# Kernel tuning notes

Measured on AMD Instinct MI355X. Metric: run time of the kernel, lower is better.

The kernel has to match this reference:

```python
import jax, jax.numpy as jnp
import numpy as np

B_SZ, SEQ, D_MODEL = 1, 2048, 1024
D_IN, N_STATE, DT_RANK, KSIZE = 2048, 16, 64, 3


def setup_inputs() -> dict:
    key = jax.random.key(0)
    ks = jax.random.split(key, 7)
    x = jax.random.normal(ks[0], (B_SZ, SEQ, D_MODEL), jnp.float32)
    W_in = jax.random.normal(ks[1], (D_MODEL, 2 * D_IN), jnp.float32) * 0.02
    conv_w = jax.random.normal(ks[2], (D_IN, 1, KSIZE), jnp.float32) * 0.1  # OIH, depthwise
    W_x = jax.random.normal(ks[3], (D_IN, DT_RANK + 2 * N_STATE), jnp.float32) * 0.02
    W_delta = jax.random.normal(ks[4], (DT_RANK, D_IN), jnp.float32) * 0.02
    b_delta = jnp.zeros((D_IN,), jnp.float32)
    # Keras initializer: A_log[d, n] = n+1 (arange 1..N repeated over d_in rows)
    A_log = jnp.tile(jnp.arange(1, N_STATE + 1, dtype=jnp.float32)[None, :], (D_IN, 1))
    D = jnp.ones((D_IN,), jnp.float32)
    W_out = jax.random.normal(ks[5], (D_IN, D_MODEL), jnp.float32) * 0.02
    return dict(x=x, W_in=W_in, conv_w=conv_w, W_x=W_x, W_delta=W_delta,
                b_delta=b_delta, A_log=A_log, D=D, W_out=W_out)


def selective_scan(u, delta, A, Bm, Cm, D):
    # u, delta: (b,l,d); A: (d,n); Bm, Cm: (b,l,n); D: (d,)
    dA = jnp.einsum('bld,dn->bldn', delta, A)
    dB_u = jnp.einsum('bld,bld,bln->bldn', delta, u, Bm)
    # shift dA left by one step, zero at the end (matches pad+slice in source)
    dA_shift = jnp.concatenate([dA[:, 1:], jnp.zeros_like(dA[:, :1])], axis=1)
    # reversed cumulative sum along time, then exp
    dA_cs = jnp.exp(jnp.flip(jnp.cumsum(jnp.flip(dA_shift, axis=1), axis=1), axis=1))
    xs = jnp.cumsum(dB_u * dA_cs, axis=1) / (dA_cs + 1e-12)
    y = jnp.einsum('bldn,bln->bld', xs, Cm)
    return y + u * D


def reference(x, W_in, conv_w, W_x, W_delta, b_delta, A_log, D, W_out):
    d_in = conv_w.shape[0]
    ksz = conv_w.shape[2]
    n = A_log.shape[1]
    dtr = W_delta.shape[0]
    x_and_res = x @ W_in                       # (b,l,2*d_in)
    xi, res = x_and_res[..., :d_in], x_and_res[..., d_in:]
    # depthwise causal conv over time (channels_first with left padding k-1)
    xc = jnp.transpose(xi, (0, 2, 1))          # (b,d_in,l)
    xc = jax.lax.conv_general_dilated(
        xc, conv_w, window_strides=(1,), padding=[(ksz - 1, 0)],
        dimension_numbers=('NCH', 'OIH', 'NCH'), feature_group_count=d_in)
    xi = jnp.transpose(xc, (0, 2, 1))          # (b,l,d_in)
    xi = xi * jax.nn.sigmoid(xi)               # swish
    # SSM
    A = -jnp.exp(A_log)
    x_dbl = xi @ W_x                           # (b,l,dtr+2n)
    delta_lr = x_dbl[..., :dtr]
    Bm = x_dbl[..., dtr:dtr + n]
    Cm = x_dbl[..., dtr + n:]
    delta = jax.nn.softplus(delta_lr @ W_delta + b_delta)
    y = selective_scan(xi, delta, A, Bm, Cm, D)
    y = y * (res * jax.nn.sigmoid(res))
    return y @ W_out
```

## Files before the change

### kernel.cpp

```cpp
#include <hip/hip_runtime.h>
#include <hip/hip_bf16.h>
#include <math.h>

#define SEQ     2048
#define D_MODEL 1024
#define D_IN    2048
#define N_STATE 16
#define DT_RANK 64
#define XDBL_W  96
#define XDBL_LD 128
#define LC      64
#define NCH     32
#define DT      32
#define WX_KSPLIT 16
#define WX_KSEG   (D_IN / WX_KSPLIT)
#define OUT_KSPLIT 4
#define OUT_KSEG   (D_IN / OUT_KSPLIT)

#define LOG2E   1.4426950408889634f

typedef __attribute__((ext_vector_type(8))) _Float16 f16x8;
typedef __attribute__((ext_vector_type(4))) float f32x4;

__device__ __forceinline__ float fast_exp2(float x) { return __builtin_amdgcn_exp2f(x); }
__device__ __forceinline__ float fast_rcp(float x)  { return __builtin_amdgcn_rcpf(x); }

__device__ __forceinline__ ushort f2h(float x) {
    _Float16 h = (_Float16)x;
    return __builtin_bit_cast(ushort, h);
}
__device__ __forceinline__ float h2f(ushort u) {
    return (float)__builtin_bit_cast(_Float16, u);
}

__device__ __forceinline__ void gload16(const ushort* g, ushort* l) {
    __builtin_amdgcn_global_load_lds(
        (const __attribute__((address_space(1))) void*)g,
        (__attribute__((address_space(3))) void*)l, 16, 0, 0);
}

#define GL_DEFS                                                                \
    const int lane8 = lane >> 3;                                               \
    const int scol  = (lane & 7) ^ lane8;                                      \
    const int wq    = wave * 8;

#define STAGE_GL(SRC, DST, BASE, LDK, KOFF)                                    \
    _Pragma("unroll")                                                          \
    for (int q = 0; q < 4; ++q) {                                              \
        const int rr = q * 32 + wq + lane8;                                    \
        gload16(&SRC[(size_t)((BASE) + rr) * (LDK) + (KOFF) + scol * 8],       \
                ((ushort*)DST) + (q * 256 + wave * 64) * 8);                   \
    }

#define COMPUTE_KS(KS)                                                         \
    {                                                                          \
        const int slot = ((((KS) << 2) | l4) ^ sw) * 8;                        \
        f16x8 ah[4], al[4], bb[4];                                             \
        _Pragma("unroll")                                                      \
        for (int f = 0; f < 4; ++f) {                                          \
            const int ar = mw + f * 16 + l15;                                  \
            const int br = nw + f * 16 + l15;                                  \
            ah[f] = *(const f16x8*)&lA[0][ar][slot];                           \
            al[f] = *(const f16x8*)&lA[1][ar][slot];                           \
            bb[f] = *(const f16x8*)&lB[br][slot];                              \
        }                                                                      \
        _Pragma("unroll")                                                      \
        for (int i = 0; i < 4; ++i)                                            \
            _Pragma("unroll")                                                  \
            for (int j = 0; j < 4; ++j) {                                      \
                acc[i][j] = __builtin_amdgcn_mfma_f32_16x16x32_f16(            \
                    ah[i], bb[j], acc[i][j], 0, 0, 0);                         \
                acc[i][j] = __builtin_amdgcn_mfma_f32_16x16x32_f16(            \
                    al[i], bb[j], acc[i][j], 0, 0, 0);                         \
            }                                                                  \
    }

template <int CTRL>
__device__ __forceinline__ float dpp_add(float x) {
    int y = __builtin_amdgcn_update_dpp(0, __float_as_int(x), CTRL, 0xF, 0xF, true);
    return x + __int_as_float(y);
}

__global__ __launch_bounds__(256) void split_f16(
    const float* __restrict__ in, ushort* __restrict__ hi,
    ushort* __restrict__ lo)
{
    const int i = blockIdx.x * 256 + threadIdx.x;
    const float4 v = *(const float4*)&in[(size_t)i * 4];
    ushort4 h, l;
    h.x = f2h(v.x); l.x = f2h(v.x - h2f(h.x));
    h.y = f2h(v.y); l.y = f2h(v.y - h2f(h.y));
    h.z = f2h(v.z); l.z = f2h(v.z - h2f(h.z));
    h.w = f2h(v.w); l.w = f2h(v.w - h2f(h.w));
    *(ushort4*)&hi[(size_t)i * 4] = h;
    *(ushort4*)&lo[(size_t)i * 4] = l;
}

__global__ __launch_bounds__(256) void trans_f16(
    const float* __restrict__ in, ushort* __restrict__ out, int R, int C)
{
    __shared__ float tile[32][33];
    const int c0 = blockIdx.x * 32;
    const int r0 = blockIdx.y * 32;
    const int tc = threadIdx.x & 31;
    const int tr = threadIdx.x >> 5;
#pragma unroll
    for (int q = 0; q < 4; ++q)
        tile[tr + 8 * q][tc] = in[(size_t)(r0 + tr + 8 * q) * C + c0 + tc];
    __syncthreads();
#pragma unroll
    for (int q = 0; q < 4; ++q)
        out[(size_t)(c0 + tr + 8 * q) * R + r0 + tc] = f2h(tile[tc][tr + 8 * q]);
}

__global__ __launch_bounds__(256) void trans_f16_pad(
    const float* __restrict__ in, ushort* __restrict__ out, int R, int Csrc)
{
    __shared__ float tile[32][33];
    const int c0 = blockIdx.x * 32;
    const int r0 = blockIdx.y * 32;
    const int tc = threadIdx.x & 31;
    const int tr = threadIdx.x >> 5;
#pragma unroll
    for (int q = 0; q < 4; ++q) {
        const int c = c0 + tc;
        tile[tr + 8 * q][tc] =
            (c < Csrc) ? in[(size_t)(r0 + tr + 8 * q) * Csrc + c] : 0.f;
    }
    __syncthreads();
#pragma unroll
    for (int q = 0; q < 4; ++q)
        out[(size_t)(c0 + tr + 8 * q) * R + r0 + tc] = f2h(tile[tc][tr + 8 * q]);
}

__global__ __launch_bounds__(256) void gemm_mfma3(
    const ushort* __restrict__ Ahi, const ushort* __restrict__ Alo,
    const ushort* __restrict__ Bf,
    float* __restrict__ C0, float* __restrict__ C1, int nsplit,
    int M, int N, int K, int ldc0, int ldc1)
{
    __shared__ ushort lA[2][128][64];
    __shared__ ushort lB[128][64];

    const int t    = threadIdx.x;
    const int m0   = blockIdx.y * 128;
    const int n0   = blockIdx.x * 128;
    const int wave = t >> 6;
    const int lane = t & 63;
    const int mw   = (wave & 1) * 64;
    const int nw   = (wave >> 1) * 64;
    const int l15  = lane & 15;
    const int l4   = lane >> 4;
    const int sw   = l15 & 7;
    GL_DEFS

    f32x4 acc[4][4];
#pragma unroll
    for (int i = 0; i < 4; ++i)
#pragma unroll
        for (int j = 0; j < 4; ++j)
            acc[i][j] = (f32x4){0.f, 0.f, 0.f, 0.f};

    for (int k0 = 0; k0 < K; k0 += 64) {
        __syncthreads();
        STAGE_GL(Ahi, lA[0], m0, K, k0)
        STAGE_GL(Alo, lA[1], m0, K, k0)
        STAGE_GL(Bf,  lB,    n0, K, k0)
        __syncthreads();
        COMPUTE_KS(0)
        COMPUTE_KS(1)
    }

#pragma unroll
    for (int i = 0; i < 4; ++i) {
        const int rowg = m0 + mw + i * 16 + l4 * 4;
#pragma unroll
        for (int j = 0; j < 4; ++j) {
            const int colg = n0 + nw + j * 16 + l15;
            if (colg < nsplit) {
#pragma unroll
                for (int v = 0; v < 4; ++v)
                    C0[(size_t)(rowg + v) * ldc0 + colg] = acc[i][j][v];
            } else {
                const int cc = colg - nsplit;
#pragma unroll
                for (int v = 0; v < 4; ++v) {
                    const float r = acc[i][j][v];
                    C1[(size_t)(rowg + v) * ldc1 + cc] =
                        r * fast_rcp(1.f + fast_exp2(-LOG2E * r));
                }
            }
        }
    }
}

__global__ __launch_bounds__(256) void gemm_wx_mfma(
    const ushort* __restrict__ Ahi, const ushort* __restrict__ Alo,
    const ushort* __restrict__ Bf, float* __restrict__ part)
{
    __shared__ ushort lA[2][128][64];
    __shared__ ushort lB[128][64];

    const int t    = threadIdx.x;
    const int kb   = blockIdx.x;
    const int m0   = blockIdx.y * 128;
    const int wave = t >> 6;
    const int lane = t & 63;
    const int mw   = (wave & 1) * 64;
    const int nw   = (wave >> 1) * 64;
    const int l15  = lane & 15;
    const int l4   = lane >> 4;
    const int sw   = l15 & 7;
    const int kbase = kb * WX_KSEG;
    GL_DEFS

    f32x4 acc[4][4];
#pragma unroll
    for (int i = 0; i < 4; ++i)
#pragma unroll
        for (int j = 0; j < 4; ++j)
            acc[i][j] = (f32x4){0.f, 0.f, 0.f, 0.f};

    for (int k0 = 0; k0 < WX_KSEG; k0 += 64) {
        __syncthreads();
        STAGE_GL(Ahi, lA[0], m0, D_IN, kbase + k0)
        STAGE_GL(Alo, lA[1], m0, D_IN, kbase + k0)
        STAGE_GL(Bf,  lB,    0,  D_IN, kbase + k0)
        __syncthreads();
        COMPUTE_KS(0)
        COMPUTE_KS(1)
    }

#pragma unroll
    for (int i = 0; i < 4; ++i) {
        const int rowg = m0 + mw + i * 16 + l4 * 4;
#pragma unroll
        for (int j = 0; j < 4; ++j) {
            const int colg = nw + j * 16 + l15;
#pragma unroll
            for (int v = 0; v < 4; ++v)
                part[((size_t)kb * SEQ + rowg + v) * XDBL_LD + colg] =
                    acc[i][j][v];
        }
    }
}

__global__ __launch_bounds__(256) void wx_reduce(
    const float* __restrict__ part, float* __restrict__ xdbl)
{
    const size_t i = (size_t)(blockIdx.x * 256 + threadIdx.x) * 4;
    float4 s = *(const float4*)&part[i];
#pragma unroll
    for (int kb = 1; kb < WX_KSPLIT; ++kb) {
        const float4 v = *(const float4*)&part[(size_t)kb * SEQ * XDBL_LD + i];
        s.x += v.x; s.y += v.y; s.z += v.z; s.w += v.w;
    }
    *(float4*)&xdbl[i] = s;
}

__global__ __launch_bounds__(256) void gemm_out_mfma(
    const ushort* __restrict__ Ahi, const ushort* __restrict__ Alo,
    const ushort* __restrict__ Bf,
    float* __restrict__ p01, float* __restrict__ p23)
{
    __shared__ ushort lA[2][128][64];
    __shared__ ushort lB[128][64];

    const int t    = threadIdx.x;
    const int n0   = blockIdx.x * 128;
    const int m0   = blockIdx.y * 128;
    const int kb   = blockIdx.z;
    const int wave = t >> 6;
    const int lane = t & 63;
    const int mw   = (wave & 1) * 64;
    const int nw   = (wave >> 1) * 64;
    const int l15  = lane & 15;
    const int l4   = lane >> 4;
    const int sw   = l15 & 7;
    const int kbase = kb * OUT_KSEG;
    GL_DEFS

    f32x4 acc[4][4];
#pragma unroll
    for (int i = 0; i < 4; ++i)
#pragma unroll
        for (int j = 0; j < 4; ++j)
            acc[i][j] = (f32x4){0.f, 0.f, 0.f, 0.f};

    for (int k0 = 0; k0 < OUT_KSEG; k0 += 64) {
        __syncthreads();
        STAGE_GL(Ahi, lA[0], m0, D_IN, kbase + k0)
        STAGE_GL(Alo, lA[1], m0, D_IN, kbase + k0)
        STAGE_GL(Bf,  lB,    n0, D_IN, kbase + k0)
        __syncthreads();
        COMPUTE_KS(0)
        COMPUTE_KS(1)
    }

    float* base = (kb & 2) ? p23 : p01;
    base += (size_t)(kb & 1) * SEQ * D_MODEL;
#pragma unroll
    for (int i = 0; i < 4; ++i) {
        const int rowg = m0 + mw + i * 16 + l4 * 4;
#pragma unroll
        for (int j = 0; j < 4; ++j) {
            const int colg = n0 + nw + j * 16 + l15;
#pragma unroll
            for (int v = 0; v < 4; ++v)
                base[(size_t)(rowg + v) * D_MODEL + colg] = acc[i][j][v];
        }
    }
}

__global__ __launch_bounds__(256) void out_reduce(
    const float* __restrict__ p01, const float* __restrict__ p23,
    float* __restrict__ out)
{
    const size_t i = (size_t)(blockIdx.x * 256 + threadIdx.x) * 4;
    const size_t MN = (size_t)SEQ * D_MODEL;
    const float4 a = *(const float4*)&p01[i];
    const float4 b = *(const float4*)&p01[i + MN];
    const float4 c = *(const float4*)&p23[i];
    const float4 d = *(const float4*)&p23[i + MN];
    float4 s;
    s.x = ((a.x + b.x) + c.x) + d.x;
    s.y = ((a.y + b.y) + c.y) + d.y;
    s.z = ((a.z + b.z) + c.z) + d.z;
    s.w = ((a.w + b.w) + c.w) + d.w;
    *(float4*)&out[i] = s;
}

__global__ __launch_bounds__(256) void gemm_delta64(
    const float* __restrict__ A,
    const float* __restrict__ B,
    const float* __restrict__ bias,
    float* __restrict__ C,
    double* __restrict__ csumOut)
{
    __shared__ float At[64][68];
    __shared__ float Bs[64][68];
    __shared__ double dpart[16][64];

    const int t  = threadIdx.x;
    const int n0 = blockIdx.x * 64;
    const int m0 = blockIdx.y * 64;

    {
        const int r   = t >> 2;
        const int c16 = (t & 3) * 16;
#pragma unroll
        for (int q = 0; q < 4; ++q) {
            const float4 v =
                *(const float4*)&A[(size_t)(m0 + r) * XDBL_LD + c16 + q * 4];
            At[c16 + q * 4 + 0][r] = v.x;
            At[c16 + q * 4 + 1][r] = v.y;
            At[c16 + q * 4 + 2][r] = v.z;
            At[c16 + q * 4 + 3][r] = v.w;
        }
#pragma unroll
        for (int q = 0; q < 4; ++q)
            *(float4*)&Bs[r][c16 + q * 4] =
                *(const float4*)&B[(size_t)r * D_IN + n0 + c16 + q * 4];
    }
    __syncthreads();

    const int tx = t & 15;
    const int ty = t >> 4;
    float acc[4][4];
#pragma unroll
    for (int i = 0; i < 4; ++i)
#pragma unroll
        for (int j = 0; j < 4; ++j) acc[i][j] = 0.f;

#pragma unroll 1
    for (int k0 = 0; k0 < 64; k0 += 8) {
#pragma unroll
        for (int kk = 0; kk < 8; ++kk) {
            const int k = k0 + kk;
            const float4 a = *(const float4*)&At[k][ty * 4];
            const float4 b = *(const float4*)&Bs[k][tx * 4];
            const float av[4] = {a.x, a.y, a.z, a.w};
            const float bv[4] = {b.x, b.y, b.z, b.w};
#pragma unroll
            for (int i = 0; i < 4; ++i)
#pragma unroll
                for (int j = 0; j < 4; ++j)
                    acc[i][j] = fmaf(av[i], bv[j], acc[i][j]);
        }
    }

    double dsum[4];
#pragma unroll
    for (int j = 0; j < 4; ++j) dsum[j] = 0.0;
#pragma unroll
    for (int i = 0; i < 4; ++i) {
        float vals[4];
#pragma unroll
        for (int j = 0; j < 4; ++j) {
            float v = acc[i][j] + bias[n0 + tx * 4 + j];
            v = (v > 20.f) ? v : log1pf(__expf(v));
            vals[j] = v;
            dsum[j] += (double)v;
        }
        *(float4*)&C[(size_t)(m0 + ty * 4 + i) * D_IN + n0 + tx * 4] =
            *(float4*)vals;
    }
#pragma unroll
    for (int j = 0; j < 4; ++j) dpart[ty][tx * 4 + j] = dsum[j];
    __syncthreads();
    if (t < 64) {
        double s = 0.0;
#pragma unroll
        for (int q = 0; q < 16; ++q) s += dpart[q][t];
        csumOut[(size_t)(m0 >> 6) * D_IN + n0 + t] = s;
    }
}

__global__ __launch_bounds__(256) void conv_silu_split(
    const float* __restrict__ xi, const float* __restrict__ cw,
    float* __restrict__ u, ushort* __restrict__ uhi, ushort* __restrict__ ulo)
{
    const int id = blockIdx.x * 256 + threadIdx.x;
    const int l = id >> 11;
    const int d = id & (D_IN - 1);
    const float w0 = cw[d * 3 + 0];
    const float w1 = cw[d * 3 + 1];
    const float w2 = cw[d * 3 + 2];
    const float x0  = xi[(size_t)l * D_IN + d];
    const float xm1 = (l >= 1) ? xi[(size_t)(l - 1) * D_IN + d] : 0.f;
    const float xm2 = (l >= 2) ? xi[(size_t)(l - 2) * D_IN + d] : 0.f;
    const float v = w0 * xm2 + w1 * xm1 + w2 * x0;
    const float s = fast_rcp(1.f + fast_exp2(-LOG2E * v));
    const float uu = v * s;
    u[id] = uu;
    const ushort h = f2h(uu);
    uhi[id] = h;
    ulo[id] = f2h(uu - h2f(h));
}

__global__ __launch_bounds__(256) void sfx_precompute(
    const float* __restrict__ delta, const double* __restrict__ csum,
    float* __restrict__ sfx)
{
    const int d = blockIdx.x * 256 + threadIdx.x;
    const int c = blockIdx.y;
    double S = 0.0, P = 0.0;
    for (int c2 = 0; c2 < NCH; ++c2) {
        if (c2 == c) P = S;
        S += csum[(size_t)c2 * D_IN + d];
    }
    const double T = S;
    for (int i = 0; i < LC; ++i) {
        const size_t row = (size_t)(c * LC + i) * D_IN + d;
        P += (double)delta[row];
        sfx[row] = (float)fmax(T - P, 0.0);
    }
}

__global__ __launch_bounds__(256) void scan_partA(
    const float* __restrict__ delta, const float* __restrict__ u,
    const float* __restrict__ sfxbuf, const float* __restrict__ xdbl,
    const float* __restrict__ Alog, float* __restrict__ Wc)
{
    __shared__ float2 spA[LC][DT];
    __shared__ float2 sbA[LC][8];

    const int t  = threadIdx.x;
    const int c  = blockIdx.x;
    const int d0 = blockIdx.y * DT;

#pragma unroll
    for (int q = 0; q < 8; ++q) {
        const int e = q * 256 + t;
        const int r = e >> 5, col = e & 31;
        const size_t row = (size_t)(c * LC + r) * D_IN + d0 + col;
        spA[r][col] = make_float2(delta[row] * u[row], sfxbuf[row]);
    }
#pragma unroll
    for (int q = 0; q < 2; ++q) {
        const int e = q * 256 + t;
        const int r = e >> 3, n8e = e & 7;
        const size_t base = (size_t)(c * LC + r) * XDBL_LD + DT_RANK;
        sbA[r][n8e] = make_float2(xdbl[base + n8e], xdbl[base + 8 + n8e]);
    }
    __syncthreads();

    const int dq = t >> 3;
    const int n8 = t & 7;
    const int d  = d0 + dq;
    const float An2a = -expf(Alog[d * N_STATE + n8]) * LOG2E;
    const float An2b = -expf(Alog[d * N_STATE + n8 + 8]) * LOG2E;

    float W0 = 0.f, W1 = 0.f;
#pragma unroll
    for (int i = 0; i < LC; ++i) {
        const float2 p = spA[i][dq];
        const float2 b = sbA[i][n8];
        W0 = fmaf(p.x * b.x, fast_exp2(An2a * p.y), W0);
        W1 = fmaf(p.x * b.y, fast_exp2(An2b * p.y), W1);
    }
    const size_t o = ((size_t)c * D_IN + d) * N_STATE + n8;
    Wc[o]     = W0;
    Wc[o + 8] = W1;
}

__global__ __launch_bounds__(256) void scan_combine(float* __restrict__ Wc)
{
    const int id = blockIdx.x * 256 + threadIdx.x;
    float W = 0.f;
    for (int c = 0; c < NCH; ++c) {
        const size_t idx = (size_t)c * (D_IN * N_STATE) + id;
        const float w = Wc[idx];
        Wc[idx] = W;
        W += w;
    }
}

__global__ __launch_bounds__(256) void scan_partC(
    const float* __restrict__ delta, const float* __restrict__ u,
    const float* __restrict__ xdbl, const float* __restrict__ W0buf,
    const float* __restrict__ sfxbuf, const float* __restrict__ Alog,
    const float* __restrict__ Dvec, const float* __restrict__ rgbuf,
    float* __restrict__ yg)
{
    __shared__ float4 spack[LC][DT];
    __shared__ float4 sbc[LC][8];

    const int t  = threadIdx.x;
    const int c  = blockIdx.x;
    const int d0 = blockIdx.y * DT;

#pragma unroll
    for (int q = 0; q < 8; ++q) {
        const int e = q * 256 + t;
        const int r = e >> 5, col = e & 31;
        const size_t row = (size_t)(c * LC + r) * D_IN + d0 + col;
        const float dv = delta[row];
        const float uv = u[row];
        spack[r][col] = make_float4(dv * uv, sfxbuf[row], uv, rgbuf[row]);
    }
#pragma unroll
    for (int q = 0; q < 2; ++q) {
        const int e = q * 256 + t;
        const int r = e >> 3, n8e = e & 7;
        const size_t base = (size_t)(c * LC + r) * XDBL_LD + DT_RANK;
        sbc[r][n8e] = make_float4(xdbl[base + n8e],      xdbl[base + 16 + n8e],
                                  xdbl[base + 8 + n8e],  xdbl[base + 24 + n8e]);
    }
    __syncthreads();

    const int dq = t >> 3;
    const int n8 = t & 7;
    const int d  = d0 + dq;
    const float An2a = -expf(Alog[d * N_STATE + n8]) * LOG2E;
    const float An2b = -expf(Alog[d * N_STATE + n8 + 8]) * LOG2E;
    const float Dd = Dvec[d];

    const size_t wo = ((size_t)c * D_IN + d) * N_STATE + n8;
    float W0 = W0buf[wo];
    float W1 = W0buf[wo + 8];

#pragma unroll
    for (int i = 0; i < LC; ++i) {
        const float4 p  = spack[i][dq];
        const float4 bc = sbc[i][n8];
        const float E0 = fast_exp2(An2a * p.y);
        const float E1 = fast_exp2(An2b * p.y);
        W0 = fmaf(p.x * bc.x, E0, W0);
        W1 = fmaf(p.x * bc.z, E1, W1);
        const float xs0 = W0 * fast_rcp(E0 + 1e-12f);
        const float xs1 = W1 * fast_rcp(E1 + 1e-12f);
        float contrib = fmaf(xs0, bc.y, xs1 * bc.w);
        contrib = dpp_add<0xB1>(contrib);
        contrib = dpp_add<0x4E>(contrib);
        contrib = dpp_add<0x124>(contrib);
        if (n8 == 0) {
            yg[(size_t)(c * LC + i) * D_IN + d] =
                fmaf(p.z, Dd, contrib) * p.w;
        }
    }
}

extern "C" void kernel_launch(void* const* d_in, const int* in_sizes, int n_in,
                              void* d_out, int out_size, void* d_ws, size_t ws_size,
                              hipStream_t stream)
{
    const float* x      = (const float*)d_in[0];
    const float* W_in   = (const float*)d_in[1];
    const float* conv_w = (const float*)d_in[2];
    const float* W_x    = (const float*)d_in[3];
    const float* W_del  = (const float*)d_in[4];
    const float* b_del  = (const float*)d_in[5];
    const float* A_log  = (const float*)d_in[6];
    const float* Dv     = (const float*)d_in[7];
    const float* W_out  = (const float*)d_in[8];
    float* out = (float*)d_out;

    char* ws = (char*)d_ws;
    float*  xi    = (float*)(ws + 0);
    float*  wxp   = (float*)(ws + 0);
    float*  sfx   = (float*)(ws + 0);
    ushort* yg_hi = (ushort*)(ws + 0);
    ushort* yg_lo = (ushort*)(ws + 8388608);
    float*  rg    = (float*)(ws + 16777216);
    float*  p01   = (float*)(ws + 16777216);
    ushort* x_hi  = (ushort*)(ws + 33554432);
    ushort* x_lo  = (ushort*)(ws + 37748736);
    float*  u     = (float*)(ws + 33554432);
    ushort* wo    = (ushort*)(ws + 33554432);
    float*  xdbl  = (float*)(ws + 50331648);
    ushort* wi    = (ushort*)(ws + 51380224);
    ushort* u_hi  = (ushort*)(ws + 51380224);
    ushort* u_lo  = (ushort*)(ws + 59768832);
    float*  delta = (float*)(ws + 51380224);
    float*  p23   = (float*)(ws + 51380224);
    float*  Wc    = (float*)(ws + 68157440);
    double* csum  = (double*)(ws + 72351744);
    ushort* wx    = (ushort*)(ws + 73416704);
    float*  yg    = delta;

    trans_f16<<<dim3(4096 / 32, 1024 / 32), 256, 0, stream>>>(
        W_in, wi, 1024, 4096);

    split_f16<<<(SEQ * D_MODEL / 4) / 256, 256, 0, stream>>>(x, x_hi, x_lo);

    gemm_mfma3<<<dim3(4096 / 128, 2048 / 128), 256, 0, stream>>>(
        x_hi, x_lo, wi, xi, rg, D_IN,
        SEQ, 2 * D_IN, D_MODEL, D_IN, D_IN);

    conv_silu_split<<<(SEQ * D_IN) / 256, 256, 0, stream>>>(
        xi, conv_w, u, u_hi, u_lo);

    trans_f16_pad<<<dim3(XDBL_LD / 32, D_IN / 32), 256, 0, stream>>>(
        W_x, wx, D_IN, XDBL_W);

    gemm_wx_mfma<<<dim3(WX_KSPLIT, SEQ / 128), 256, 0, stream>>>(
        u_hi, u_lo, wx, wxp);
    wx_reduce<<<(SEQ * XDBL_LD / 4) / 256, 256, 0, stream>>>(wxp, xdbl);

    gemm_delta64<<<dim3(2048 / 64, 2048 / 64), 256, 0, stream>>>(
        xdbl, W_del, b_del, delta, csum);

    sfx_precompute<<<dim3(D_IN / 256, NCH), 256, 0, stream>>>(delta, csum, sfx);

    scan_partA<<<dim3(NCH, D_IN / DT), 256, 0, stream>>>(
        delta, u, sfx, xdbl, A_log, Wc);
    scan_combine<<<(D_IN * N_STATE) / 256, 256, 0, stream>>>(Wc);
    scan_partC<<<dim3(NCH, D_IN / DT), 256, 0, stream>>>(
        delta, u, xdbl, Wc, sfx, A_log, Dv, rg, yg);

    split_f16<<<(SEQ * D_IN / 4) / 256, 256, 0, stream>>>(yg, yg_hi, yg_lo);

    trans_f16<<<dim3(1024 / 32, 2048 / 32), 256, 0, stream>>>(
        W_out, wo, 2048, 1024);

    gemm_out_mfma<<<dim3(D_MODEL / 128, SEQ / 128, OUT_KSPLIT), 256, 0, stream>>>(
        yg_hi, yg_lo, wo, p01, p23);
    out_reduce<<<(SEQ * D_MODEL / 4) / 256, 256, 0, stream>>>(p01, p23, out);
}
```

Baseline: 215.2 us.

## Fuse suffix-sum precompute into scan kernels and emit split f16 output directly

Removes the separate sfx_precompute kernel and instead recomputes the per-chunk suffix sum of delta inside both scan_partA and scan_partC, working from shared memory with 32 threads per block doing a serial double-precision pass. scan_partC now writes the gated output directly as hi/lo f16 halves, which removes the split_f16 launch and the full fp32 yg round trip. This saves two launches and a large sfx buffer write and read, but adds a serial 64-step double-precision loop on only 32 threads per block, plus an extra barrier, and that loop runs twice (once in each scan kernel).

After: 207.6 us, median of 2. 3.6% less time.

```diff
diff --git a/kernel.cpp b/kernel.cpp
--- a/kernel.cpp
+++ b/kernel.cpp
@@ -438,28 +438,9 @@
     ulo[id] = f2h(uu - h2f(h));
 }
 
-__global__ __launch_bounds__(256) void sfx_precompute(
-    const float* __restrict__ delta, const double* __restrict__ csum,
-    float* __restrict__ sfx)
-{
-    const int d = blockIdx.x * 256 + threadIdx.x;
-    const int c = blockIdx.y;
-    double S = 0.0, P = 0.0;
-    for (int c2 = 0; c2 < NCH; ++c2) {
-        if (c2 == c) P = S;
-        S += csum[(size_t)c2 * D_IN + d];
-    }
-    const double T = S;
-    for (int i = 0; i < LC; ++i) {
-        const size_t row = (size_t)(c * LC + i) * D_IN + d;
-        P += (double)delta[row];
-        sfx[row] = (float)fmax(T - P, 0.0);
-    }
-}
-
 __global__ __launch_bounds__(256) void scan_partA(
     const float* __restrict__ delta, const float* __restrict__ u,
-    const float* __restrict__ sfxbuf, const float* __restrict__ xdbl,
+    const double* __restrict__ csum, const float* __restrict__ xdbl,
     const float* __restrict__ Alog, float* __restrict__ Wc)
 {
     __shared__ float2 spA[LC][DT];
@@ -474,7 +455,8 @@
         const int e = q * 256 + t;
         const int r = e >> 5, col = e & 31;
         const size_t row = (size_t)(c * LC + r) * D_IN + d0 + col;
-        spA[r][col] = make_float2(delta[row] * u[row], sfxbuf[row]);
+        const float dv = delta[row];
+        spA[r][col] = make_float2(dv * u[row], dv);
     }
 #pragma unroll
     for (int q = 0; q < 2; ++q) {
@@ -482,6 +464,20 @@
         const int r = e >> 3, n8e = e & 7;
         const size_t base = (size_t)(c * LC + r) * XDBL_LD + DT_RANK;
         sbA[r][n8e] = make_float2(xdbl[base + n8e], xdbl[base + 8 + n8e]);
+    }
+    __syncthreads();
+
+    if (t < DT) {
+        const int d = d0 + t;
+        double S = 0.0, P = 0.0;
+        for (int c2 = 0; c2 < NCH; ++c2) {
+            if (c2 == c) P = S;
+            S += csum[(size_t)c2 * D_IN + d];
+        }
+        for (int i = 0; i < LC; ++i) {
+            P += (double)spA[i][t].y;
+            spA[i][t].y = (float)fmax(S - P, 0.0);
+        }
     }
     __syncthreads();
 
@@ -519,9 +515,9 @@
 __global__ __launch_bounds__(256) void scan_partC(
     const float* __restrict__ delta, const float* __restrict__ u,
     const float* __restrict__ xdbl, const float* __restrict__ W0buf,
-    const float* __restrict__ sfxbuf, const float* __restrict__ Alog,
+    const double* __restrict__ csum, const float* __restrict__ Alog,
     const float* __restrict__ Dvec, const float* __restrict__ rgbuf,
-    float* __restrict__ yg)
+    ushort* __restrict__ ygh, ushort* __restrict__ ygl)
 {
     __shared__ float4 spack[LC][DT];
     __shared__ float4 sbc[LC][8];
@@ -537,7 +533,7 @@
         const size_t row = (size_t)(c * LC + r) * D_IN + d0 + col;
         const float dv = delta[row];
         const float uv = u[row];
-        spack[r][col] = make_float4(dv * uv, sfxbuf[row], uv, rgbuf[row]);
+        spack[r][col] = make_float4(dv * uv, dv, uv, rgbuf[row]);
     }
 #pragma unroll
     for (int q = 0; q < 2; ++q) {
@@ -546,6 +542,20 @@
         const size_t base = (size_t)(c * LC + r) * XDBL_LD + DT_RANK;
         sbc[r][n8e] = make_float4(xdbl[base + n8e],      xdbl[base + 16 + n8e],
                                   xdbl[base + 8 + n8e],  xdbl[base + 24 + n8e]);
+    }
+    __syncthreads();
+
+    if (t < DT) {
+        const int d = d0 + t;
+        double S = 0.0, P = 0.0;
+        for (int c2 = 0; c2 < NCH; ++c2) {
+            if (c2 == c) P = S;
+            S += csum[(size_t)c2 * D_IN + d];
+        }
+        for (int i = 0; i < LC; ++i) {
+            P += (double)spack[i][t].y;
+            spack[i][t].y = (float)fmax(S - P, 0.0);
+        }
     }
     __syncthreads();
 
@@ -575,8 +585,11 @@
         contrib = dpp_add<0x4E>(contrib);
         contrib = dpp_add<0x124>(contrib);
         if (n8 == 0) {
-            yg[(size_t)(c * LC + i) * D_IN + d] =
-                fmaf(p.z, Dd, contrib) * p.w;
+            const float ygv = fmaf(p.z, Dd, contrib) * p.w;
+            const size_t row = (size_t)(c * LC + i) * D_IN + d;
+            const ushort h = f2h(ygv);
+            ygh[row] = h;
+            ygl[row] = f2h(ygv - h2f(h));
         }
     }
 }
@@ -599,7 +612,6 @@
     char* ws = (char*)d_ws;
     float*  xi    = (float*)(ws + 0);
     float*  wxp   = (float*)(ws + 0);
-    float*  sfx   = (float*)(ws + 0);
     ushort* yg_hi = (ushort*)(ws + 0);
     ushort* yg_lo = (ushort*)(ws + 8388608);
     float*  rg    = (float*)(ws + 16777216);
@@ -617,7 +629,6 @@
     float*  Wc    = (float*)(ws + 68157440);
     double* csum  = (double*)(ws + 72351744);
     ushort* wx    = (ushort*)(ws + 73416704);
-    float*  yg    = delta;
 
     trans_f16<<<dim3(4096 / 32, 1024 / 32), 256, 0, stream>>>(
         W_in, wi, 1024, 4096);
@@ -641,15 +652,11 @@
     gemm_delta64<<<dim3(2048 / 64, 2048 / 64), 256, 0, stream>>>(
         xdbl, W_del, b_del, delta, csum);
 
-    sfx_precompute<<<dim3(D_IN / 256, NCH), 256, 0, stream>>>(delta, csum, sfx);
-
     scan_partA<<<dim3(NCH, D_IN / DT), 256, 0, stream>>>(
-        delta, u, sfx, xdbl, A_log, Wc);
+        delta, u, csum, xdbl, A_log, Wc);
     scan_combine<<<(D_IN * N_STATE) / 256, 256, 0, stream>>>(Wc);
     scan_partC<<<dim3(NCH, D_IN / DT), 256, 0, stream>>>(
-        delta, u, xdbl, Wc, sfx, A_log, Dv, rg, yg);
-
-    split_f16<<<(SEQ * D_IN / 4) / 256, 256, 0, stream>>>(yg, yg_hi, yg_lo);
+        delta, u, xdbl, Wc, csum, A_log, Dv, rg, yg_hi, yg_lo);
 
     trans_f16<<<dim3(1024 / 32, 2048 / 32), 256, 0, stream>>>(
         W_out, wo, 2048, 1024);
```
